# Performance work log

Hardware: AMD Instinct MI355X
Metric: run time of the kernel (lower is better)

## Reference

```python
import jax, jax.numpy as jnp
import numpy as np

N = 100000
E = 1600000
D = 128


def setup_inputs() -> dict:
    key = jax.random.key(0)
    ks = jax.random.split(key, 9)
    s = 1.0 / np.sqrt(D)
    return {
        "x": jax.random.normal(ks[0], (N, D), dtype=jnp.float32),
        "edge_index": jax.random.randint(ks[1], (2, E), 0, N, dtype=jnp.int64),
        # SAGEConv layer 1: lin_l (neighbor path, with bias), lin_r (root path, no bias)
        "Wl1": jax.random.normal(ks[2], (D, D), dtype=jnp.float32) * s,
        "bl1": jnp.zeros((D,), dtype=jnp.float32),
        "Wr1": jax.random.normal(ks[3], (D, D), dtype=jnp.float32) * s,
        # SAGEConv layer 2
        "Wl2": jax.random.normal(ks[4], (D, D), dtype=jnp.float32) * s,
        "bl2": jnp.zeros((D,), dtype=jnp.float32),
        "Wr2": jax.random.normal(ks[5], (D, D), dtype=jnp.float32) * s,
    }


def _sage_conv(x, src, dst, Wl, bl, Wr):
    # PyG SAGEConv, aggr='mean', root_weight=True:
    #   out = lin_l(mean_{j in N(i)} x_j) + lin_r(x_i)
    msg = x[src]                                              # [E, D] gather
    agg = jax.ops.segment_sum(msg, dst, num_segments=N)       # [N, D]
    cnt = jax.ops.segment_sum(jnp.ones((src.shape[0],), x.dtype), dst, num_segments=N)
    agg = agg / jnp.maximum(cnt, 1.0)[:, None]                # mean aggregation
    return agg @ Wl.T + bl + x @ Wr.T


def reference(x, edge_index, Wl1, bl1, Wr1, Wl2, bl2, Wr2):
    src, dst = edge_index[0], edge_index[1]
    h = jax.nn.relu(_sage_conv(x, src, dst, Wl1, bl1, Wr1))
    out = _sage_conv(h, src, dst, Wl2, bl2, Wr2)
    return out
```

## Files before the change

### kernel.cpp

```cpp
#include <hip/hip_runtime.h>
#include <stdint.h>

#define DN 128
#define NBITS 6
#define BNODES 64
#define HB 2048
#define NSL 64
#define NLOC 256

__host__ __device__ static inline int divup(int a, int b){ return (a+b-1)/b; }

typedef __attribute__((ext_vector_type(8))) short bf16x8;
typedef __attribute__((ext_vector_type(4))) float floatx4;

__device__ __forceinline__ unsigned short f2bf(float f){
  unsigned int x = __float_as_uint(f);
  unsigned int r = x + 0x7fffu + ((x >> 16) & 1u);
  return (unsigned short)(r >> 16);
}
__device__ __forceinline__ unsigned int pack2(unsigned short a, unsigned short b){
  return (unsigned int)a | ((unsigned int)b << 16);
}


__global__ __launch_bounds__(256)
void hist_pass(const int* __restrict__ dst, int* __restrict__ gHist, int E){
  __shared__ int h[NLOC];
  int p = blockIdx.x & 7, s = blockIdx.x >> 3;
  int t = threadIdx.x;
  h[t] = 0;
  __syncthreads();
  int n4 = E >> 2, per4 = divup(n4, NSL);
  int lo = s*per4, hi = min(lo+per4, n4);
  const int4* dst4 = (const int4*)dst;
  for (int i = lo + t; i < hi; i += 256){
    int4 d4 = dst4[i];
    int dd[4] = {d4.x, d4.y, d4.z, d4.w};
    #pragma unroll
    for (int j=0;j<4;j++){
      int b = dd[j] >> NBITS;
      if ((b & 7) == p) atomicAdd(&h[b>>3], 1);
    }
  }
  if (s == NSL-1){
    for (int e = (n4<<2) + t; e < E; e += 256){
      int b = dst[e] >> NBITS;
      if ((b & 7) == p) atomicAdd(&h[b>>3], 1);
    }
  }
  __syncthreads();
  gHist[blockIdx.x*NLOC + t] = h[t];
}

__global__ __launch_bounds__(256)
void scan_offsets(const int* __restrict__ gHist, int* __restrict__ blockOffset,
                  int* __restrict__ bucketTotal){
  int b = blockIdx.x*4 + (threadIdx.x >> 6);
  int k = threadIdx.x & 63;
  int p = b & 7, lb = b >> 3;
  int idx = (k*8 + p)*NLOC + lb;
  int v = gHist[idx];
  int sft = v;
  #pragma unroll
  for (int off=1; off<64; off<<=1){
    int u = __shfl_up(sft, off, 64);
    if (k >= off) sft += u;
  }
  blockOffset[idx] = sft - v;
  if (k == 63) bucketTotal[b] = sft;
}

__global__ __launch_bounds__(256)
void bucket_base(const int* __restrict__ bucketTotal, int* __restrict__ bucketBase){
  __shared__ int s[256];
  int t = threadIdx.x;
  int v[8]; int sum = 0;
  #pragma unroll
  for (int j=0;j<8;j++){ v[j] = bucketTotal[t*8+j]; sum += v[j]; }
  s[t] = sum; __syncthreads();
  for (int off=1; off<256; off<<=1){
    int y = (t>=off)? s[t-off] : 0;
    __syncthreads();
    s[t] += y;
    __syncthreads();
  }
  int excl = s[t] - sum;
  #pragma unroll
  for (int j=0;j<8;j++){ bucketBase[t*8+j] = excl; excl += v[j]; }
  if (t == 255) bucketBase[HB] = excl;
}

__global__ __launch_bounds__(256)
void scatter_pass(const int* __restrict__ src, const int* __restrict__ dst,
                  const int* __restrict__ bucketBase, const int* __restrict__ blockOffset,
                  unsigned int* __restrict__ packed, int E){
  __shared__ int cur[NLOC];
  int p = blockIdx.x & 7, s = blockIdx.x >> 3;
  int t = threadIdx.x;
  cur[t] = bucketBase[(t<<3)|p] + blockOffset[blockIdx.x*NLOC + t];
  __syncthreads();
  int n4 = E >> 2, per4 = divup(n4, NSL);
  int lo = s*per4, hi = min(lo+per4, n4);
  const int4* dst4 = (const int4*)dst;
  const int4* src4 = (const int4*)src;
  for (int i = lo + t; i < hi; i += 256){
    int4 d4 = dst4[i];
    int4 s4 = src4[i];
    int dd[4] = {d4.x, d4.y, d4.z, d4.w};
    int ss[4] = {s4.x, s4.y, s4.z, s4.w};
    #pragma unroll
    for (int j=0;j<4;j++){
      int d = dd[j], b = d >> NBITS;
      if ((b & 7) == p){
        int pos = atomicAdd(&cur[b>>3], 1);
        packed[pos] = (unsigned)ss[j] | ((unsigned)(d & (BNODES-1)) << 17);
      }
    }
  }
  if (s == NSL-1){
    for (int e = (n4<<2) + t; e < E; e += 256){
      int d = dst[e], b = d >> NBITS;
      if ((b & 7) == p){
        int pos = atomicAdd(&cur[b>>3], 1);
        packed[pos] = (unsigned)src[e] | ((unsigned)(d & (BNODES-1)) << 17);
      }
    }
  }
}

__global__ __launch_bounds__(256)
void node_sort(const int* __restrict__ bucketBase, const unsigned int* __restrict__ packed,
               int* __restrict__ csr_src, int* __restrict__ nodeOff, int n){
  __shared__ int cnts[BNODES], offs[BNODES+1], cursor[BNODES];
  int b = blockIdx.x, t = threadIdx.x;
  int beg = bucketBase[b], end = bucketBase[b+1], cnt = end - beg;
  if (t < BNODES) cnts[t] = 0;
  __syncthreads();
  for (int i=t; i<cnt; i+=256) atomicAdd(&cnts[(packed[beg+i]>>17)&63], 1);
  __syncthreads();
  if (t < BNODES){
    int v = cnts[t], sft = v;
    #pragma unroll
    for (int off=1; off<64; off<<=1){
      int u = __shfl_up(sft, off, 64);
      if (t >= off) sft += u;
    }
    offs[t] = sft - v; cursor[t] = sft - v;
    if (t == 63) offs[BNODES] = sft;
  }
  __syncthreads();
  for (int i=t; i<cnt; i+=256){
    unsigned pk = packed[beg+i];
    int nd = (pk>>17)&63;
    int r = atomicAdd(&cursor[nd], 1);
    csr_src[beg + r] = (int)(pk & 0x1FFFFu);
  }
  if (t <= BNODES){
    int node = b*BNODES + t;
    if (node <= n) nodeOff[node] = beg + offs[t];
  }
}


__global__ __launch_bounds__(256)
void convert_x_kernel(const float* __restrict__ src, unsigned short* __restrict__ dst, int count8){
  int i = blockIdx.x*256 + threadIdx.x;
  if (i >= count8) return;
  const float4* s = (const float4*)src + (size_t)i*2;
  float4 a = s[0], b = s[1];
  uint4 o;
  o.x = pack2(f2bf(a.x), f2bf(a.y));
  o.y = pack2(f2bf(a.z), f2bf(a.w));
  o.z = pack2(f2bf(b.x), f2bf(b.y));
  o.w = pack2(f2bf(b.z), f2bf(b.w));
  ((uint4*)dst)[i] = o;
}

__global__ __launch_bounds__(256)
void convert_w_kernel(const float* __restrict__ w0, const float* __restrict__ w1,
                      const float* __restrict__ w2, const float* __restrict__ w3,
                      unsigned short* __restrict__ dst){
  int tid = blockIdx.x*256 + threadIdx.x;
  if (tid >= 8192) return;
  int mat = tid >> 11, off = tid & 2047;
  const float* w = (mat==0)?w0:(mat==1)?w1:(mat==2)?w2:w3;
  const float4* s = (const float4*)w + (size_t)off*2;
  float4 a = s[0], b = s[1];
  uint4 o;
  o.x = pack2(f2bf(a.x), f2bf(a.y));
  o.y = pack2(f2bf(a.z), f2bf(a.w));
  o.z = pack2(f2bf(b.x), f2bf(b.y));
  o.w = pack2(f2bf(b.z), f2bf(b.w));
  ((uint4*)(dst + (size_t)mat*16384))[off] = o;
}

__global__ __launch_bounds__(256)
void aggregate_csr(const unsigned short* __restrict__ xb, const int* __restrict__ nodeOff,
                   const int* __restrict__ csr_src, unsigned short* __restrict__ aggb, int n){
  int g = (blockIdx.x*256 + threadIdx.x) >> 4;
  int l = threadIdx.x & 15;
  if (g >= n) return;
  int beg = nodeOff[g], end = nodeOff[g+1];
  float acc[8] = {0,0,0,0,0,0,0,0};
  #define ACCUM(u) { unsigned int w;                                   \
      w=(u).x; acc[0]+=__uint_as_float(w<<16); acc[1]+=__uint_as_float(w&0xffff0000u); \
      w=(u).y; acc[2]+=__uint_as_float(w<<16); acc[3]+=__uint_as_float(w&0xffff0000u); \
      w=(u).z; acc[4]+=__uint_as_float(w<<16); acc[5]+=__uint_as_float(w&0xffff0000u); \
      w=(u).w; acc[6]+=__uint_as_float(w<<16); acc[7]+=__uint_as_float(w&0xffff0000u); }
  int p = beg;
  for (; p+4 <= end; p += 4){
    int s0 = csr_src[p], s1 = csr_src[p+1], s2 = csr_src[p+2], s3 = csr_src[p+3];
    uint4 u0 = ((const uint4*)(xb + (size_t)s0*DN))[l];
    uint4 u1 = ((const uint4*)(xb + (size_t)s1*DN))[l];
    uint4 u2 = ((const uint4*)(xb + (size_t)s2*DN))[l];
    uint4 u3 = ((const uint4*)(xb + (size_t)s3*DN))[l];
    ACCUM(u0) ACCUM(u1) ACCUM(u2) ACCUM(u3)
  }
  for (; p < end; ++p){
    int s0 = csr_src[p];
    uint4 u0 = ((const uint4*)(xb + (size_t)s0*DN))[l];
    ACCUM(u0)
  }
  #undef ACCUM
  float inv = 1.f / fmaxf((float)(end-beg), 1.f);
  uint4 o;
  o.x = pack2(f2bf(acc[0]*inv), f2bf(acc[1]*inv));
  o.y = pack2(f2bf(acc[2]*inv), f2bf(acc[3]*inv));
  o.z = pack2(f2bf(acc[4]*inv), f2bf(acc[5]*inv));
  o.w = pack2(f2bf(acc[6]*inv), f2bf(acc[7]*inv));
  ((uint4*)(aggb + (size_t)g*DN))[l] = o;
}

template<bool RELU, bool OUT_BF16>
__global__ __launch_bounds__(256)
void gemm_mfma(const unsigned short* __restrict__ A1, const unsigned short* __restrict__ W1b,
               const unsigned short* __restrict__ A2, const unsigned short* __restrict__ W2b,
               const float* __restrict__ bias, void* __restrict__ out,
               int rt_total, int rt_per_block)
{
  int wave = threadIdx.x >> 6;
  int lane = threadIdx.x & 63;
  int m = lane & 15, quad = lane >> 4;

  bf16x8 Bf[2][2][4];
  {
    const unsigned short* Ws[2] = {W1b, W2b};
    #pragma unroll
    for (int c2=0;c2<2;c2++){
      int col = wave*32 + c2*16 + m;
      #pragma unroll
      for (int mat=0;mat<2;mat++){
        const unsigned short* wrow = Ws[mat] + (size_t)col*DN + quad*8;
        #pragma unroll
        for (int kc=0;kc<4;kc++)
          Bf[c2][mat][kc] = *(const bf16x8*)(wrow + kc*32);
      }
    }
  }
  float bv0 = bias[wave*32 + m];
  float bv1 = bias[wave*32 + 16 + m];

  int rt_begin = blockIdx.x * rt_per_block;
  int rt_end = rt_begin + rt_per_block; if (rt_end > rt_total) rt_end = rt_total;

  for (int rt = rt_begin; rt < rt_end; ++rt){
    const unsigned short* a1p = A1 + ((size_t)(rt*16 + m))*DN + quad*8;
    const unsigned short* a2p = A2 + ((size_t)(rt*16 + m))*DN + quad*8;
    bf16x8 Af[2][4];
    #pragma unroll
    for (int kc=0;kc<4;kc++){
      Af[0][kc] = *(const bf16x8*)(a1p + kc*32);
      Af[1][kc] = *(const bf16x8*)(a2p + kc*32);
    }
    __syncthreads();
    floatx4 acc0 = {0.f,0.f,0.f,0.f}, acc1 = {0.f,0.f,0.f,0.f};
    #pragma unroll
    for (int mat=0; mat<2; mat++)
      #pragma unroll
      for (int kc=0; kc<4; kc++){
        acc0 = __builtin_amdgcn_mfma_f32_16x16x32_bf16(Af[mat][kc], Bf[0][mat][kc], acc0, 0,0,0);
        acc1 = __builtin_amdgcn_mfma_f32_16x16x32_bf16(Af[mat][kc], Bf[1][mat][kc], acc1, 0,0,0);
      }
    #pragma unroll
    for (int r=0;r<4;r++){
      int row = rt*16 + quad*4 + r;
      float v0 = acc0[r] + bv0;
      float v1 = acc1[r] + bv1;
      if (RELU){ v0 = fmaxf(v0, 0.f); v1 = fmaxf(v1, 0.f); }
      if (OUT_BF16){
        unsigned short* o = (unsigned short*)out + (size_t)row*DN + wave*32 + m;
        o[0]  = f2bf(v0);
        o[16] = f2bf(v1);
      } else {
        float* o = (float*)out + (size_t)row*DN + wave*32 + m;
        o[0]  = v0;
        o[16] = v1;
      }
    }
  }
}


extern "C" void kernel_launch(void* const* d_in, const int* in_sizes, int n_in,
                              void* d_out, int out_size, void* d_ws, size_t ws_size,
                              hipStream_t stream) {
  const float* x   = (const float*)d_in[0];
  const int*   ei  = (const int*)d_in[1];
  const float* Wl1 = (const float*)d_in[2];
  const float* bl1 = (const float*)d_in[3];
  const float* Wr1 = (const float*)d_in[4];
  const float* Wl2 = (const float*)d_in[5];
  const float* bl2 = (const float*)d_in[6];
  const float* Wr2 = (const float*)d_in[7];

  const int n = in_sizes[0] / DN;
  const int E = in_sizes[1] / 2;
  const int* src = ei;
  const int* dst = ei + E;

  char* ws = (char*)d_ws;
  char* ws_end = ws + ws_size;
  int* gHist       = (int*)ws;  ws += (size_t)NSL*8*NLOC*4;
  int* blockOffset = (int*)ws;  ws += (size_t)NSL*8*NLOC*4;
  int* bucketTotal = (int*)ws;  ws += (size_t)HB*4;
  int* bucketBase  = (int*)ws;  ws += (size_t)(HB+1)*4;
  ws = (char*)(((uintptr_t)ws + 255) & ~(uintptr_t)255);
  unsigned int* packed = (unsigned int*)ws; ws += (size_t)E*4;
  int* csr_src     = (int*)ws;  ws += (size_t)E*4;
  int* nodeOff     = (int*)ws;  ws += (size_t)(n+1)*4;
  ws = (char*)(((uintptr_t)ws + 255) & ~(uintptr_t)255);
  unsigned short* Wb   = (unsigned short*)ws; ws += 4*16384*2;
  unsigned short* xb   = (unsigned short*)ws; ws += (size_t)n*DN*2;
  unsigned short* aggb = (unsigned short*)ws; ws += (size_t)n*DN*2;
  unsigned short* hb = xb;
  if (ws + (size_t)n*DN*2 <= ws_end) { hb = (unsigned short*)ws; ws += (size_t)n*DN*2; }

  unsigned short* Wl1b = Wb;
  unsigned short* Wr1b = Wb + 16384;
  unsigned short* Wl2b = Wb + 2*16384;
  unsigned short* Wr2b = Wb + 3*16384;

  hist_pass   <<<NSL*8, 256,0,stream>>>(dst, gHist, E);
  scan_offsets<<<HB/4,  256,0,stream>>>(gHist, blockOffset, bucketTotal);
  bucket_base <<<1,     256,0,stream>>>(bucketTotal, bucketBase);
  scatter_pass<<<NSL*8, 256,0,stream>>>(src, dst, bucketBase, blockOffset, packed, E);
  node_sort   <<<HB,    256,0,stream>>>(bucketBase, packed, csr_src, nodeOff, n);

  convert_x_kernel<<<divup(n*DN/8,256),256,0,stream>>>(x, xb, n*DN/8);
  convert_w_kernel<<<32,256,0,stream>>>(Wl1, Wr1, Wl2, Wr2, Wb);

  const int rt_total = n / 16;
  const int rt_per_block = 5;
  const int gblocks = divup(rt_total, rt_per_block);
  const int agrid = divup(n*16, 256);

  aggregate_csr<<<agrid,256,0,stream>>>(xb, nodeOff, csr_src, aggb, n);
  gemm_mfma<true, true><<<gblocks,256,0,stream>>>(aggb, Wl1b, xb, Wr1b, bl1, hb, rt_total, rt_per_block);
  aggregate_csr<<<agrid,256,0,stream>>>(hb, nodeOff, csr_src, aggb, n);
  gemm_mfma<false,false><<<gblocks,256,0,stream>>>(aggb, Wl2b, hb, Wr2b, bl2, d_out, rt_total, rt_per_block);
}
```

Before: 359.2 us.

## Use full per-block bucket histograms in counting sort and merge convert kernels

Replaces the 8-way partitioned histogram and scatter, where each block re-read its slice of edges and kept only one eighth of the buckets, with 128 blocks that each keep a full 2048-bucket shared histogram. Each edge is now read once per pass instead of eight times. The scan kernel is reworked to handle 128 slices per bucket using two wave scans. The x and weight bf16 conversion kernels are merged into one launch. The trade-off is fewer blocks in the hist and scatter passes, more shared memory per block, and denser LDS atomic contention.

```diff
diff --git a/kernel.cpp b/kernel.cpp
--- a/kernel.cpp
+++ b/kernel.cpp
@@ -5,8 +5,7 @@
 #define NBITS 6
 #define BNODES 64
 #define HB 2048
-#define NSL 64
-#define NLOC 256
+#define NSL 128
 
 __host__ __device__ static inline int divup(int a, int b){ return (a+b-1)/b; }
 
@@ -25,31 +24,26 @@
 
 __global__ __launch_bounds__(256)
 void hist_pass(const int* __restrict__ dst, int* __restrict__ gHist, int E){
-  __shared__ int h[NLOC];
-  int p = blockIdx.x & 7, s = blockIdx.x >> 3;
-  int t = threadIdx.x;
-  h[t] = 0;
+  __shared__ int h[HB];
+  int s = blockIdx.x, t = threadIdx.x;
+  for (int i=t; i<HB; i+=256) h[i] = 0;
   __syncthreads();
   int n4 = E >> 2, per4 = divup(n4, NSL);
   int lo = s*per4, hi = min(lo+per4, n4);
   const int4* dst4 = (const int4*)dst;
   for (int i = lo + t; i < hi; i += 256){
     int4 d4 = dst4[i];
-    int dd[4] = {d4.x, d4.y, d4.z, d4.w};
-    #pragma unroll
-    for (int j=0;j<4;j++){
-      int b = dd[j] >> NBITS;
-      if ((b & 7) == p) atomicAdd(&h[b>>3], 1);
-    }
+    atomicAdd(&h[d4.x >> NBITS], 1);
+    atomicAdd(&h[d4.y >> NBITS], 1);
+    atomicAdd(&h[d4.z >> NBITS], 1);
+    atomicAdd(&h[d4.w >> NBITS], 1);
   }
   if (s == NSL-1){
-    for (int e = (n4<<2) + t; e < E; e += 256){
-      int b = dst[e] >> NBITS;
-      if ((b & 7) == p) atomicAdd(&h[b>>3], 1);
-    }
-  }
-  __syncthreads();
-  gHist[blockIdx.x*NLOC + t] = h[t];
+    for (int e = (n4<<2) + t; e < E; e += 256)
+      atomicAdd(&h[dst[e] >> NBITS], 1);
+  }
+  __syncthreads();
+  for (int i=t; i<HB; i+=256) gHist[s*HB + i] = h[i];
 }
 
 __global__ __launch_bounds__(256)
@@ -57,17 +51,19 @@
                   int* __restrict__ bucketTotal){
   int b = blockIdx.x*4 + (threadIdx.x >> 6);
   int k = threadIdx.x & 63;
-  int p = b & 7, lb = b >> 3;
-  int idx = (k*8 + p)*NLOC + lb;
-  int v = gHist[idx];
-  int sft = v;
+  int v0 = gHist[(size_t)k*HB + b];
+  int v1 = gHist[(size_t)(k+64)*HB + b];
+  int s0 = v0, s1 = v1;
   #pragma unroll
   for (int off=1; off<64; off<<=1){
-    int u = __shfl_up(sft, off, 64);
-    if (k >= off) sft += u;
-  }
-  blockOffset[idx] = sft - v;
-  if (k == 63) bucketTotal[b] = sft;
+    int u0 = __shfl_up(s0, off, 64);
+    int u1 = __shfl_up(s1, off, 64);
+    if (k >= off){ s0 += u0; s1 += u1; }
+  }
+  int t0 = __shfl(s0, 63, 64);
+  blockOffset[(size_t)k*HB + b]      = s0 - v0;
+  blockOffset[(size_t)(k+64)*HB + b] = t0 + s1 - v1;
+  if (k == 63) bucketTotal[b] = t0 + s1;
 }
 
 __global__ __launch_bounds__(256)
@@ -94,10 +90,10 @@
 void scatter_pass(const int* __restrict__ src, const int* __restrict__ dst,
                   const int* __restrict__ bucketBase, const int* __restrict__ blockOffset,
                   unsigned int* __restrict__ packed, int E){
-  __shared__ int cur[NLOC];
-  int p = blockIdx.x & 7, s = blockIdx.x >> 3;
-  int t = threadIdx.x;
-  cur[t] = bucketBase[(t<<3)|p] + blockOffset[blockIdx.x*NLOC + t];
+  __shared__ int cur[HB];
+  int s = blockIdx.x, t = threadIdx.x;
+  for (int i=t; i<HB; i+=256)
+    cur[i] = bucketBase[i] + blockOffset[(size_t)s*HB + i];
   __syncthreads();
   int n4 = E >> 2, per4 = divup(n4, NSL);
   int lo = s*per4, hi = min(lo+per4, n4);
@@ -110,20 +106,16 @@
     int ss[4] = {s4.x, s4.y, s4.z, s4.w};
     #pragma unroll
     for (int j=0;j<4;j++){
-      int d = dd[j], b = d >> NBITS;
-      if ((b & 7) == p){
-        int pos = atomicAdd(&cur[b>>3], 1);
-        packed[pos] = (unsigned)ss[j] | ((unsigned)(d & (BNODES-1)) << 17);
-      }
+      int d = dd[j];
+      int pos = atomicAdd(&cur[d >> NBITS], 1);
+      packed[pos] = (unsigned)ss[j] | ((unsigned)(d & (BNODES-1)) << 17);
     }
   }
   if (s == NSL-1){
     for (int e = (n4<<2) + t; e < E; e += 256){
-      int d = dst[e], b = d >> NBITS;
-      if ((b & 7) == p){
-        int pos = atomicAdd(&cur[b>>3], 1);
-        packed[pos] = (unsigned)src[e] | ((unsigned)(d & (BNODES-1)) << 17);
-      }
+      int d = dst[e];
+      int pos = atomicAdd(&cur[d >> NBITS], 1);
+      packed[pos] = (unsigned)src[e] | ((unsigned)(d & (BNODES-1)) << 17);
     }
   }
 }
@@ -163,35 +155,29 @@
 
 
 __global__ __launch_bounds__(256)
-void convert_x_kernel(const float* __restrict__ src, unsigned short* __restrict__ dst, int count8){
+void convert_all(const float* __restrict__ x,
+                 const float* __restrict__ w0, const float* __restrict__ w1,
+                 const float* __restrict__ w2, const float* __restrict__ w3,
+                 unsigned short* __restrict__ xb, unsigned short* __restrict__ Wb,
+                 int count8){
   int i = blockIdx.x*256 + threadIdx.x;
-  if (i >= count8) return;
-  const float4* s = (const float4*)src + (size_t)i*2;
+  const float* sp; unsigned short* dp; int off;
+  if (i < count8){ sp = x; dp = xb; off = i; }
+  else {
+    int tid = i - count8;
+    if (tid >= 8192) return;
+    int mat = tid >> 11; off = tid & 2047;
+    sp = (mat==0)?w0:(mat==1)?w1:(mat==2)?w2:w3;
+    dp = Wb + (size_t)mat*16384;
+  }
+  const float4* s = (const float4*)sp + (size_t)off*2;
   float4 a = s[0], b = s[1];
   uint4 o;
   o.x = pack2(f2bf(a.x), f2bf(a.y));
   o.y = pack2(f2bf(a.z), f2bf(a.w));
   o.z = pack2(f2bf(b.x), f2bf(b.y));
   o.w = pack2(f2bf(b.z), f2bf(b.w));
-  ((uint4*)dst)[i] = o;
-}
-
-__global__ __launch_bounds__(256)
-void convert_w_kernel(const float* __restrict__ w0, const float* __restrict__ w1,
-                      const float* __restrict__ w2, const float* __restrict__ w3,
-                      unsigned short* __restrict__ dst){
-  int tid = blockIdx.x*256 + threadIdx.x;
-  if (tid >= 8192) return;
-  int mat = tid >> 11, off = tid & 2047;
-  const float* w = (mat==0)?w0:(mat==1)?w1:(mat==2)?w2:w3;
-  const float4* s = (const float4*)w + (size_t)off*2;
-  float4 a = s[0], b = s[1];
-  uint4 o;
-  o.x = pack2(f2bf(a.x), f2bf(a.y));
-  o.y = pack2(f2bf(a.z), f2bf(a.w));
-  o.z = pack2(f2bf(b.x), f2bf(b.y));
-  o.w = pack2(f2bf(b.z), f2bf(b.w));
-  ((uint4*)(dst + (size_t)mat*16384))[off] = o;
+  ((uint4*)dp)[off] = o;
 }
 
 __global__ __launch_bounds__(256)
@@ -320,8 +306,8 @@
 
   char* ws = (char*)d_ws;
   char* ws_end = ws + ws_size;
-  int* gHist       = (int*)ws;  ws += (size_t)NSL*8*NLOC*4;
-  int* blockOffset = (int*)ws;  ws += (size_t)NSL*8*NLOC*4;
+  int* gHist       = (int*)ws;  ws += (size_t)NSL*HB*4;
+  int* blockOffset = (int*)ws;  ws += (size_t)NSL*HB*4;
   int* bucketTotal = (int*)ws;  ws += (size_t)HB*4;
   int* bucketBase  = (int*)ws;  ws += (size_t)(HB+1)*4;
   ws = (char*)(((uintptr_t)ws + 255) & ~(uintptr_t)255);
@@ -340,14 +326,14 @@
   unsigned short* Wl2b = Wb + 2*16384;
   unsigned short* Wr2b = Wb + 3*16384;
 
-  hist_pass   <<<NSL*8, 256,0,stream>>>(dst, gHist, E);
-  scan_offsets<<<HB/4,  256,0,stream>>>(gHist, blockOffset, bucketTotal);
-  bucket_base <<<1,     256,0,stream>>>(bucketTotal, bucketBase);
-  scatter_pass<<<NSL*8, 256,0,stream>>>(src, dst, bucketBase, blockOffset, packed, E);
-  node_sort   <<<HB,    256,0,stream>>>(bucketBase, packed, csr_src, nodeOff, n);
-
-  convert_x_kernel<<<divup(n*DN/8,256),256,0,stream>>>(x, xb, n*DN/8);
-  convert_w_kernel<<<32,256,0,stream>>>(Wl1, Wr1, Wl2, Wr2, Wb);
+  hist_pass   <<<NSL,  256,0,stream>>>(dst, gHist, E);
+  scan_offsets<<<HB/4, 256,0,stream>>>(gHist, blockOffset, bucketTotal);
+  bucket_base <<<1,    256,0,stream>>>(bucketTotal, bucketBase);
+  scatter_pass<<<NSL,  256,0,stream>>>(src, dst, bucketBase, blockOffset, packed, E);
+  node_sort   <<<HB,   256,0,stream>>>(bucketBase, packed, csr_src, nodeOff, n);
+
+  const int count8 = n*DN/8;
+  convert_all<<<divup(count8 + 8192, 256),256,0,stream>>>(x, Wl1, Wr1, Wl2, Wr2, xb, Wb, count8);
 
   const int rt_total = n / 16;
   const int rt_per_block = 5;
@@ -355,7 +341,7 @@
   const int agrid = divup(n*16, 256);
 
   aggregate_csr<<<agrid,256,0,stream>>>(xb, nodeOff, csr_src, aggb, n);
-  gemm_mfma<true, true><<<gblocks,256,0,stream>>>(aggb, Wl1b, xb, Wr1b, bl1, hb, rt_total, rt_per_block);
+  gemm_mfma<true, true ><<<gblocks,256,0,stream>>>(aggb, Wl1b, xb, Wr1b, bl1, hb, rt_total, rt_per_block);
   aggregate_csr<<<agrid,256,0,stream>>>(hb, nodeOff, csr_src, aggb, n);
   gemm_mfma<false,false><<<gblocks,256,0,stream>>>(aggb, Wl2b, hb, Wr2b, bl2, d_out, rt_total, rt_per_block);
 }
```

After: 357.5 us. No clear change (-0.4%).
